# Kernel optimization log

Hardware: AMD Instinct MI355X
Metric: run time of the kernel (lower is better)

Reference implementation:

```python
import jax, jax.numpy as jnp
import numpy as np

N = 100000   # mesh points
n = 32       # latent dim
K = 32       # neighbours per point
M = 16       # clusters
MU = 1.0


def setup_inputs() -> dict:
    key = jax.random.key(0)
    ks = jax.random.split(key, 8)
    x = jax.random.normal(ks[0], (N,), jnp.float32)
    enc_w = jax.random.normal(ks[1], (n, N), jnp.float32) * 0.01
    enc_b = jnp.zeros((n,), jnp.float32)
    decoder = jax.random.normal(ks[2], (n, N), jnp.float32) * 0.02
    bw_w = jax.random.normal(ks[3], (n * M, n), jnp.float32) * 0.05
    bw_b = jnp.ones((n * M,), jnp.float32)  # keep bandwidths away from 0
    neighbour_distance = jax.random.uniform(ks[4], (N, K), jnp.float32, minval=0.05, maxval=1.0)
    neighbour_id = jax.random.randint(ks[5], (N, K), 0, N)
    clustering_labels = jax.random.randint(ks[6], (N,), 0, M)
    return {
        "x": x, "enc_w": enc_w, "enc_b": enc_b, "decoder": decoder,
        "bw_w": bw_w, "bw_b": bw_b,
        "neighbour_distance": neighbour_distance,
        "neighbour_id": neighbour_id,
        "clustering_labels": clustering_labels,
    }


def reference(x, enc_w, enc_b, decoder, bw_w, bw_b,
              neighbour_distance, neighbour_id, clustering_labels):
    # encode: Linear(N -> n) on a single vector
    encoded = enc_w @ x + enc_b                             # [n]
    # per-(basis, cluster) bandwidths, broadcast to points via labels
    bandwidths = (bw_w @ encoded + bw_b).reshape(n, M)      # [n, M]
    w = bandwidths[:, clustering_labels]                    # [n, N]
    # bubble window: relu(1 - d^2 / (w*mu)^2), shape [n, N, K]
    window = jax.nn.relu(1.0 - neighbour_distance[None, :, :] ** 2
                         / (w[:, :, None] * MU) ** 2)
    # NOTE: original normalizes over dim=1 (the N-points axis) — faithful here
    window = window / jnp.sum(window, axis=1, keepdims=True)
    # gather decoder rows at neighbours and reduce over neighbour axis
    convolved = jnp.sum(decoder[:, neighbour_id] * window, axis=-1)  # [n, N]
    return encoded @ convolved                              # [N]
```

## Files before the change

### kernel.cpp

```cpp
#include <hip/hip_runtime.h>

#define NPTS 100000
#define NCH 32
#define KNB 32
#define MCL 16

constexpr int IB1  = 128;
constexpr int SBLK = 512;

constexpr size_t OFF_SPART    = 0;
constexpr size_t OFF_ENC      = 4194304;
constexpr size_t OFF_INVW2    = OFF_ENC + 256;
constexpr size_t OFF_INVS     = OFF_INVW2 + 2048;
constexpr size_t OFF_SACC     = OFF_INVS + 4096;
constexpr size_t OFF_GT       = OFF_SACC + 8192;

__global__ __launch_bounds__(256) void k_enc_partial(
    const float* __restrict__ x, const float* __restrict__ enc_w,
    double* __restrict__ part, double* __restrict__ Sacc) {
  int tid = threadIdx.x;
  if (blockIdx.x == 0) {
    for (int q = tid; q < 1024; q += 256) Sacc[q] = 0.0;
  }
  int jg = blockIdx.x & 3;
  int ib = blockIdx.x >> 2;
  int j0 = jg * 8;
  double acc[8];
#pragma unroll
  for (int jj = 0; jj < 8; ++jj) acc[jj] = 0.0;
  for (int i = ib * 256 + tid; i < NPTS; i += IB1 * 256) {
    float xv = x[i];
#pragma unroll
    for (int jj = 0; jj < 8; ++jj)
      acc[jj] += (double)enc_w[(size_t)(j0 + jj) * NPTS + i] * (double)xv;
  }
#pragma unroll
  for (int jj = 0; jj < 8; ++jj) {
    double v = acc[jj];
#pragma unroll
    for (int off = 32; off >= 1; off >>= 1) v += __shfl_down(v, off);
    acc[jj] = v;
  }
  __shared__ double sw[4][8];
  int lane = tid & 63, w = tid >> 6;
  if (lane == 0)
    for (int jj = 0; jj < 8; ++jj) sw[w][jj] = acc[jj];
  __syncthreads();
  if (tid < 8) {
    double s = sw[0][tid] + sw[1][tid] + sw[2][tid] + sw[3][tid];
    part[(size_t)(j0 + tid) * IB1 + ib] = s;
  }
}

__global__ __launch_bounds__(512) void k_head(
    const double* __restrict__ part, const float* __restrict__ enc_b,
    const float* __restrict__ bw_w, const float* __restrict__ bw_b,
    double* __restrict__ enc_out, float* __restrict__ invw2) {
  __shared__ double es[32];
  __shared__ double sred[32][16];
  int tid = threadIdx.x;
  int j = tid >> 4, slot = tid & 15;
  double s = 0.0;
#pragma unroll
  for (int r = 0; r < 8; ++r) s += part[j * 128 + slot * 8 + r];
  sred[j][slot] = s;
  __syncthreads();
  if (tid < 32) {
    double t = 0.0;
    for (int q = 0; q < 16; ++q) t += sred[tid][q];
    t += (double)enc_b[tid];
    enc_out[tid] = t;
    es[tid] = t;
  }
  __syncthreads();
  double wd = 0.0;
  for (int c = 0; c < 32; ++c) wd += (double)bw_w[tid * 32 + c] * es[c];
  wd += (double)bw_b[tid];
  int jr = tid >> 4, m = tid & 15;
  invw2[m * 32 + jr] = (float)(1.0 / (wd * wd));
}

__global__ __launch_bounds__(256) void k_gt(
    const float* __restrict__ decoder, const double* __restrict__ enc,
    float* __restrict__ gT) {
  __shared__ float tile[32][33];
  __shared__ float ef[32];
  int tx = threadIdx.x & 31, ty = threadIdx.x >> 5;
  if (threadIdx.x < 32) ef[threadIdx.x] = (float)enc[threadIdx.x];
  int i0 = blockIdx.x * 32;
  for (int jj = ty; jj < 32; jj += 8)
    tile[tx][jj] = decoder[(size_t)jj * NPTS + i0 + tx];
  __syncthreads();
  for (int ii = ty; ii < 32; ii += 8)
    gT[(size_t)(i0 + ii) * 32 + tx] = tile[ii][tx] * ef[tx];
}

__global__ __launch_bounds__(256) void k_spart(
    const float* __restrict__ nd, const int* __restrict__ labels,
    const float* __restrict__ invw2, double* __restrict__ spart) {
  int tid = threadIdx.x;
  int j = tid >> 3, kq = tid & 7;
  double a0 = 0.0, a1 = 0.0, a2 = 0.0, a3 = 0.0;
  int i = blockIdx.x;
  while (i < NPTS) {
    float t0 = 0.0f, t1 = 0.0f, t2 = 0.0f, t3 = 0.0f;
#pragma unroll 4
    for (int c = 0; c < 16 && i < NPTS; ++c, i += SBLK) {
      int lab = labels[i];
      float icv = invw2[lab * 32 + j];
      float4 d = *(const float4*)&nd[(size_t)i * 32 + kq * 4];
      t0 += fmaxf(fmaf(-(d.x * d.x), icv, 1.0f), 0.0f);
      t1 += fmaxf(fmaf(-(d.y * d.y), icv, 1.0f), 0.0f);
      t2 += fmaxf(fmaf(-(d.z * d.z), icv, 1.0f), 0.0f);
      t3 += fmaxf(fmaf(-(d.w * d.w), icv, 1.0f), 0.0f);
    }
    a0 += (double)t0; a1 += (double)t1; a2 += (double)t2; a3 += (double)t3;
  }
  size_t base = (size_t)blockIdx.x * 1024 + j * 32 + kq * 4;
  spart[base + 0] = a0;
  spart[base + 1] = a1;
  spart[base + 2] = a2;
  spart[base + 3] = a3;
}

__global__ __launch_bounds__(256) void k_sred2(
    const double* __restrict__ spart, double* __restrict__ Sacc) {
  int gt = blockIdx.x * 256 + threadIdx.x;
  int jk = gt & 1023;
  int seg = gt >> 10;
  double s = 0.0;
#pragma unroll 8
  for (int r = 0; r < 32; ++r)
    s += spart[(size_t)(seg * 32 + r) * 1024 + jk];
  unsafeAtomicAdd(&Sacc[jk], s);
}

__global__ __launch_bounds__(1024) void k_sinv(
    const double* __restrict__ Sacc, float* __restrict__ invS) {
  int t = threadIdx.x;
  int j = t >> 5, k = t & 31;
  invS[k * 32 + j] = (float)(1.0 / Sacc[t]);
}

__global__ __launch_bounds__(256, 3) void k_main(
    const float* __restrict__ nd, const int* __restrict__ nid,
    const int* __restrict__ labels, const float* __restrict__ gT,
    const float* __restrict__ invw2, const float* __restrict__ invS,
    float* __restrict__ out) {
  int tid = threadIdx.x;
  int lane = tid & 63;
  int w = tid >> 6;
  int q = lane & 7;
  int g = lane >> 3;
  int wv = blockIdx.x * 4 + w;

  int id[4][4];
  float dvv[4][4];
  int lab[4];
#pragma unroll
  for (int p = 0; p < 4; ++p) {
    int i = wv + p * 25000;
    lab[p] = labels[i];
    int base = i * 32;
#pragma unroll
    for (int kk = 0; kk < 4; ++kk) {
      id[p][kk] = nid[base + kk * 8 + g];
      dvv[p][kk] = nd[base + kk * 8 + g];
    }
  }
  float4 gv[4][4];
#pragma unroll
  for (int p = 0; p < 4; ++p)
#pragma unroll
    for (int kk = 0; kk < 4; ++kk)
      gv[p][kk] = *(const float4*)&gT[(size_t)id[p][kk] * 32 + q * 4];
  float4 iwv[4];
#pragma unroll
  for (int p = 0; p < 4; ++p)
    iwv[p] = *(const float4*)&invw2[lab[p] * 32 + q * 4];
  float4 sv[4];
#pragma unroll
  for (int kk = 0; kk < 4; ++kk)
    sv[kk] = *(const float4*)&invS[(kk * 8 + g) * 32 + q * 4];

  double a[4] = {0.0, 0.0, 0.0, 0.0};
#pragma unroll
  for (int p = 0; p < 4; ++p) {
#pragma unroll
    for (int kk = 0; kk < 4; ++kk) {
      float md = -dvv[p][kk] * dvv[p][kk];
      float u0 = fmaxf(fmaf(md, iwv[p].x, 1.0f), 0.0f);
      float u1 = fmaxf(fmaf(md, iwv[p].y, 1.0f), 0.0f);
      float u2 = fmaxf(fmaf(md, iwv[p].z, 1.0f), 0.0f);
      float u3 = fmaxf(fmaf(md, iwv[p].w, 1.0f), 0.0f);
      a[p] += (double)(gv[p][kk].x * (u0 * sv[kk].x));
      a[p] += (double)(gv[p][kk].y * (u1 * sv[kk].y));
      a[p] += (double)(gv[p][kk].z * (u2 * sv[kk].z));
      a[p] += (double)(gv[p][kk].w * (u3 * sv[kk].w));
    }
  }
#pragma unroll
  for (int off = 32; off >= 1; off >>= 1) {
#pragma unroll
    for (int p = 0; p < 4; ++p) a[p] += __shfl_down(a[p], off);
  }
  if (lane == 0) {
#pragma unroll
    for (int p = 0; p < 4; ++p) out[wv + p * 25000] = (float)a[p];
  }
}

extern "C" void kernel_launch(void* const* d_in, const int* in_sizes, int n_in,
                              void* d_out, int out_size, void* d_ws,
                              size_t ws_size, hipStream_t stream) {
  const float* x       = (const float*)d_in[0];
  const float* enc_w   = (const float*)d_in[1];
  const float* enc_b   = (const float*)d_in[2];
  const float* decoder = (const float*)d_in[3];
  const float* bw_w    = (const float*)d_in[4];
  const float* bw_b    = (const float*)d_in[5];
  const float* nd      = (const float*)d_in[6];
  const int*   nid     = (const int*)d_in[7];
  const int*   labels  = (const int*)d_in[8];
  float* out = (float*)d_out;

  char* ws = (char*)d_ws;
  double* spart = (double*)(ws + OFF_SPART);
  double* part  = (double*)(ws + OFF_SPART);
  double* enc_d = (double*)(ws + OFF_ENC);
  float*  invw2 = (float*)(ws + OFF_INVW2);
  float*  invS  = (float*)(ws + OFF_INVS);
  double* Sacc  = (double*)(ws + OFF_SACC);
  float*  gT    = (float*)(ws + OFF_GT);

  hipLaunchKernelGGL(k_enc_partial, dim3(512), dim3(256), 0, stream, x, enc_w, part, Sacc);
  hipLaunchKernelGGL(k_head, dim3(1), dim3(512), 0, stream, part, enc_b, bw_w, bw_b, enc_d, invw2);
  hipLaunchKernelGGL(k_gt, dim3(3125), dim3(256), 0, stream, decoder, enc_d, gT);
  hipLaunchKernelGGL(k_spart, dim3(SBLK), dim3(256), 0, stream, nd, labels, invw2, spart);
  hipLaunchKernelGGL(k_sred2, dim3(64), dim3(256), 0, stream, spart, Sacc);
  hipLaunchKernelGGL(k_sinv, dim3(1), dim3(1024), 0, stream, Sacc, invS);
  hipLaunchKernelGGL(k_main, dim3(6250), dim3(256), 0, stream, nd, nid, labels, gT, invw2, invS, out);
}
```

Before: 199.1 us.

## Fuse gT/spart kernels, store gT in fp16, fold invS into main kernel

```diff
diff --git a/kernel.cpp b/kernel.cpp
--- a/kernel.cpp
+++ b/kernel.cpp
@@ -1,19 +1,20 @@
 #include <hip/hip_runtime.h>
 
 #define NPTS 100000
-#define NCH 32
-#define KNB 32
-#define MCL 16
 
 constexpr int IB1  = 128;
-constexpr int SBLK = 512;
-
-constexpr size_t OFF_SPART    = 0;
-constexpr size_t OFF_ENC      = 4194304;
-constexpr size_t OFF_INVW2    = OFF_ENC + 256;
-constexpr size_t OFF_INVS     = OFF_INVW2 + 2048;
-constexpr size_t OFF_SACC     = OFF_INVS + 4096;
-constexpr size_t OFF_GT       = OFF_SACC + 8192;
+constexpr int SPB2 = 1536;
+constexpr int GTB  = 3125;
+
+typedef _Float16 half_t;
+typedef _Float16 half4 __attribute__((ext_vector_type(4)));
+
+constexpr size_t OFF_PART   = 0;
+constexpr size_t OFF_ENC    = 32768;
+constexpr size_t OFF_INVW2  = 33024;
+constexpr size_t OFF_SACC   = 35072;
+constexpr size_t OFF_SPARTF = 43264;
+constexpr size_t OFF_GTH    = 6334720;
 
 __global__ __launch_bounds__(256) void k_enc_partial(
     const float* __restrict__ x, const float* __restrict__ enc_w,
@@ -80,74 +81,77 @@
   invw2[m * 32 + jr] = (float)(1.0 / (wd * wd));
 }
 
-__global__ __launch_bounds__(256) void k_gt(
+__global__ __launch_bounds__(256) void k_gtspart(
     const float* __restrict__ decoder, const double* __restrict__ enc,
-    float* __restrict__ gT) {
-  __shared__ float tile[32][33];
-  __shared__ float ef[32];
-  int tx = threadIdx.x & 31, ty = threadIdx.x >> 5;
-  if (threadIdx.x < 32) ef[threadIdx.x] = (float)enc[threadIdx.x];
-  int i0 = blockIdx.x * 32;
-  for (int jj = ty; jj < 32; jj += 8)
-    tile[tx][jj] = decoder[(size_t)jj * NPTS + i0 + tx];
-  __syncthreads();
-  for (int ii = ty; ii < 32; ii += 8)
-    gT[(size_t)(i0 + ii) * 32 + tx] = tile[ii][tx] * ef[tx];
-}
-
-__global__ __launch_bounds__(256) void k_spart(
     const float* __restrict__ nd, const int* __restrict__ labels,
-    const float* __restrict__ invw2, double* __restrict__ spart) {
-  int tid = threadIdx.x;
-  int j = tid >> 3, kq = tid & 7;
-  double a0 = 0.0, a1 = 0.0, a2 = 0.0, a3 = 0.0;
-  int i = blockIdx.x;
-  while (i < NPTS) {
+    const float* __restrict__ invw2_g, float* __restrict__ spartf,
+    half_t* __restrict__ gTh) {
+  int tid = threadIdx.x;
+  int b = blockIdx.x;
+  if (b < SPB2) {
+    __shared__ float iw[512];
+    for (int q = tid; q < 512; q += 256) iw[q] = invw2_g[q];
+    __syncthreads();
+    int j = tid >> 3, kq = tid & 7;
     float t0 = 0.0f, t1 = 0.0f, t2 = 0.0f, t3 = 0.0f;
+    int cnt = (NPTS - b + SPB2 - 1) / SPB2;
 #pragma unroll 4
-    for (int c = 0; c < 16 && i < NPTS; ++c, i += SBLK) {
+    for (int c = 0; c < cnt; ++c) {
+      int i = b + c * SPB2;
       int lab = labels[i];
-      float icv = invw2[lab * 32 + j];
+      float icv = iw[lab * 32 + j];
       float4 d = *(const float4*)&nd[(size_t)i * 32 + kq * 4];
       t0 += fmaxf(fmaf(-(d.x * d.x), icv, 1.0f), 0.0f);
       t1 += fmaxf(fmaf(-(d.y * d.y), icv, 1.0f), 0.0f);
       t2 += fmaxf(fmaf(-(d.z * d.z), icv, 1.0f), 0.0f);
       t3 += fmaxf(fmaf(-(d.w * d.w), icv, 1.0f), 0.0f);
     }
-    a0 += (double)t0; a1 += (double)t1; a2 += (double)t2; a3 += (double)t3;
-  }
-  size_t base = (size_t)blockIdx.x * 1024 + j * 32 + kq * 4;
-  spart[base + 0] = a0;
-  spart[base + 1] = a1;
-  spart[base + 2] = a2;
-  spart[base + 3] = a3;
-}
-
-__global__ __launch_bounds__(256) void k_sred2(
-    const double* __restrict__ spart, double* __restrict__ Sacc) {
+    float4 v = make_float4(t0, t1, t2, t3);
+    *(float4*)&spartf[(size_t)b * 1024 + j * 32 + kq * 4] = v;
+  } else {
+    __shared__ float tile[32][33];
+    __shared__ float ef[32];
+    int gb = b - SPB2;
+    if (tid < 32) ef[tid] = (float)enc[tid];
+    int tx = tid & 31, ty = tid >> 5;
+    int i0 = gb * 32;
+    for (int jj = ty; jj < 32; jj += 8)
+      tile[tx][jj] = decoder[(size_t)jj * NPTS + i0 + tx];
+    __syncthreads();
+    for (int ii = ty; ii < 32; ii += 8)
+      gTh[(size_t)(i0 + ii) * 32 + tx] = (half_t)(tile[ii][tx] * ef[tx]);
+  }
+}
+
+__global__ __launch_bounds__(256) void k_sred(
+    const float* __restrict__ spartf, double* __restrict__ Sacc) {
   int gt = blockIdx.x * 256 + threadIdx.x;
   int jk = gt & 1023;
   int seg = gt >> 10;
   double s = 0.0;
 #pragma unroll 8
-  for (int r = 0; r < 32; ++r)
-    s += spart[(size_t)(seg * 32 + r) * 1024 + jk];
+  for (int r = 0; r < SPB2 / 16; ++r)
+    s += (double)spartf[(size_t)(seg * (SPB2 / 16) + r) * 1024 + jk];
   unsafeAtomicAdd(&Sacc[jk], s);
 }
 
-__global__ __launch_bounds__(1024) void k_sinv(
-    const double* __restrict__ Sacc, float* __restrict__ invS) {
-  int t = threadIdx.x;
-  int j = t >> 5, k = t & 31;
-  invS[k * 32 + j] = (float)(1.0 / Sacc[t]);
-}
-
-__global__ __launch_bounds__(256, 3) void k_main(
+__global__ __launch_bounds__(256, 4) void k_main(
     const float* __restrict__ nd, const int* __restrict__ nid,
-    const int* __restrict__ labels, const float* __restrict__ gT,
-    const float* __restrict__ invw2, const float* __restrict__ invS,
+    const int* __restrict__ labels, const half_t* __restrict__ gTh,
+    const float* __restrict__ invw2_g, const double* __restrict__ Sacc,
     float* __restrict__ out) {
-  int tid = threadIdx.x;
+  __shared__ __align__(16) float iwL[512];
+  __shared__ __align__(16) float isL[1024];
+  int tid = threadIdx.x;
+#pragma unroll
+  for (int u = 0; u < 2; ++u) iwL[tid + 256 * u] = invw2_g[tid + 256 * u];
+#pragma unroll
+  for (int u = 0; u < 4; ++u) {
+    int t = tid * 4 + u;
+    int j = t >> 5, k = t & 31;
+    isL[k * 32 + j] = 1.0f / (float)Sacc[t];
+  }
+  __syncthreads();
   int lane = tid & 63;
   int w = tid >> 6;
   int q = lane & 7;
@@ -168,24 +172,25 @@
       dvv[p][kk] = nd[base + kk * 8 + g];
     }
   }
-  float4 gv[4][4];
+  half4 gv[4][4];
 #pragma unroll
   for (int p = 0; p < 4; ++p)
 #pragma unroll
     for (int kk = 0; kk < 4; ++kk)
-      gv[p][kk] = *(const float4*)&gT[(size_t)id[p][kk] * 32 + q * 4];
+      gv[p][kk] = *(const half4*)&gTh[(size_t)id[p][kk] * 32 + q * 4];
   float4 iwv[4];
 #pragma unroll
   for (int p = 0; p < 4; ++p)
-    iwv[p] = *(const float4*)&invw2[lab[p] * 32 + q * 4];
+    iwv[p] = *(const float4*)&iwL[lab[p] * 32 + q * 4];
   float4 sv[4];
 #pragma unroll
   for (int kk = 0; kk < 4; ++kk)
-    sv[kk] = *(const float4*)&invS[(kk * 8 + g) * 32 + q * 4];
-
-  double a[4] = {0.0, 0.0, 0.0, 0.0};
+    sv[kk] = *(const float4*)&isL[(kk * 8 + g) * 32 + q * 4];
+
+  double a[4];
 #pragma unroll
   for (int p = 0; p < 4; ++p) {
+    float ap = 0.0f;
 #pragma unroll
     for (int kk = 0; kk < 4; ++kk) {
       float md = -dvv[p][kk] * dvv[p][kk];
@@ -193,11 +198,12 @@
       float u1 = fmaxf(fmaf(md, iwv[p].y, 1.0f), 0.0f);
       float u2 = fmaxf(fmaf(md, iwv[p].z, 1.0f), 0.0f);
       float u3 = fmaxf(fmaf(md, iwv[p].w, 1.0f), 0.0f);
-      a[p] += (double)(gv[p][kk].x * (u0 * sv[kk].x));
-      a[p] += (double)(gv[p][kk].y * (u1 * sv[kk].y));
-      a[p] += (double)(gv[p][kk].z * (u2 * sv[kk].z));
-      a[p] += (double)(gv[p][kk].w * (u3 * sv[kk].w));
+      ap += (float)gv[p][kk].x * (u0 * sv[kk].x);
+      ap += (float)gv[p][kk].y * (u1 * sv[kk].y);
+      ap += (float)gv[p][kk].z * (u2 * sv[kk].z);
+      ap += (float)gv[p][kk].w * (u3 * sv[kk].w);
     }
+    a[p] = (double)ap;
   }
 #pragma unroll
   for (int off = 32; off >= 1; off >>= 1) {
@@ -225,19 +231,20 @@
   float* out = (float*)d_out;
 
   char* ws = (char*)d_ws;
-  double* spart = (double*)(ws + OFF_SPART);
-  double* part  = (double*)(ws + OFF_SPART);
-  double* enc_d = (double*)(ws + OFF_ENC);
-  float*  invw2 = (float*)(ws + OFF_INVW2);
-  float*  invS  = (float*)(ws + OFF_INVS);
-  double* Sacc  = (double*)(ws + OFF_SACC);
-  float*  gT    = (float*)(ws + OFF_GT);
-
-  hipLaunchKernelGGL(k_enc_partial, dim3(512), dim3(256), 0, stream, x, enc_w, part, Sacc);
-  hipLaunchKernelGGL(k_head, dim3(1), dim3(512), 0, stream, part, enc_b, bw_w, bw_b, enc_d, invw2);
-  hipLaunchKernelGGL(k_gt, dim3(3125), dim3(256), 0, stream, decoder, enc_d, gT);
-  hipLaunchKernelGGL(k_spart, dim3(SBLK), dim3(256), 0, stream, nd, labels, invw2, spart);
-  hipLaunchKernelGGL(k_sred2, dim3(64), dim3(256), 0, stream, spart, Sacc);
-  hipLaunchKernelGGL(k_sinv, dim3(1), dim3(1024), 0, stream, Sacc, invS);
-  hipLaunchKernelGGL(k_main, dim3(6250), dim3(256), 0, stream, nd, nid, labels, gT, invw2, invS, out);
-}
+  double* part   = (double*)(ws + OFF_PART);
+  double* enc_d  = (double*)(ws + OFF_ENC);
+  float*  invw2  = (float*)(ws + OFF_INVW2);
+  double* Sacc   = (double*)(ws + OFF_SACC);
+  float*  spartf = (float*)(ws + OFF_SPARTF);
+  half_t* gTh    = (half_t*)(ws + OFF_GTH);
+
+  hipLaunchKernelGGL(k_enc_partial, dim3(512), dim3(256), 0, stream,
+                     x, enc_w, part, Sacc);
+  hipLaunchKernelGGL(k_head, dim3(1), dim3(512), 0, stream,
+                     part, enc_b, bw_w, bw_b, enc_d, invw2);
+  hipLaunchKernelGGL(k_gtspart, dim3(SPB2 + GTB), dim3(256), 0, stream,
+                     decoder, enc_d, nd, labels, invw2, spartf, gTh);
+  hipLaunchKernelGGL(k_sred, dim3(64), dim3(256), 0, stream, spartf, Sacc);
+  hipLaunchKernelGGL(k_main, dim3(6250), dim3(256), 0, stream,
+                     nd, nid, labels, gTh, invw2, Sacc, out);
+}
```

Measured after the change: 161.3 us. 19.0% less time.
